# Kernel tuning notes

Measured on AMD Instinct MI355X. Metric: run time of the kernel, lower is better.

Reference implementation:

```python
import jax, jax.numpy as jnp
import numpy as np

B, N, F, D, H, L, K = 128, 128, 13, 256, 8, 8, 10
FF = 2 * D  # FFN / hidden width
HEAD = D // H


def setup_inputs() -> dict:
    key = jax.random.key(0)
    ks = iter(jax.random.split(key, 64))
    def nrm(shape, scale=0.02):
        return jax.random.normal(next(ks), shape, dtype=jnp.float32) * scale
    return {
        "input_features": jax.random.normal(next(ks), (B, N, F), dtype=jnp.float32),
        "input_points": jax.random.normal(next(ks), (B, N, 2), dtype=jnp.float32),
        "input_mask": jnp.ones((B, N, 1), dtype=jnp.float32),
        "input_time": jax.random.uniform(next(ks), (B, 1), dtype=jnp.float32),
        # get_encoding: Dense(2D, gelu) -> Dense(D, gelu)
        "enc_w1": nrm((F, FF)), "enc_b1": jnp.zeros((FF,), jnp.float32),
        "enc_w2": nrm((FF, D)), "enc_b2": jnp.zeros((D,), jnp.float32),
        # FourierProjection MLP (no bias, swish)
        "four_w1": nrm((D, FF)), "four_w2": nrm((FF, D)),
        # FiLM time projection (no bias)
        "time_w": nrm((D, FF)),
        # local KNN MLPs: round 0 input 2*F, round 1 input 2*D
        "loc1_w1": nrm((2 * F, FF)), "loc1_b1": jnp.zeros((FF,), jnp.float32),
        "loc1_w2": nrm((FF, D)), "loc1_b2": jnp.zeros((D,), jnp.float32),
        "loc2_w1": nrm((2 * D, FF)), "loc2_b1": jnp.zeros((FF,), jnp.float32),
        "loc2_w2": nrm((FF, D)), "loc2_b2": jnp.zeros((D,), jnp.float32),
        # transformer encoder layers, stacked over L
        "qkv_w": nrm((L, D, 3 * D)), "qkv_b": jnp.zeros((L, 3 * D), jnp.float32),
        "out_w": nrm((L, D, D)), "out_b": jnp.zeros((L, D), jnp.float32),
        "ln1_g": jnp.ones((L, D), jnp.float32), "ln1_b": jnp.zeros((L, D), jnp.float32),
        "ff1_w": nrm((L, D, FF)), "ff1_b": jnp.zeros((L, FF), jnp.float32),
        "ff2_w": nrm((L, FF, D)), "ff2_b": jnp.zeros((L, D), jnp.float32),
        "gamma": jnp.full((L, D), 1e-5, dtype=jnp.float32),
        "ln2_g": jnp.ones((L, D), jnp.float32), "ln2_b": jnp.zeros((L, D), jnp.float32),
    }


def _ln(x, g, b, eps=1e-5):
    m = jnp.mean(x, axis=-1, keepdims=True)
    v = jnp.var(x, axis=-1, keepdims=True)
    return (x - m) * jax.lax.rsqrt(v + eps) * g + b


def _fourier(t, w1, w2):
    # t: (B,1) -> (B,D)
    half = D // 2
    emb = np.log(10000.0) / (half - 1)
    freq = jnp.exp(-emb * jnp.arange(half, dtype=jnp.float32))
    angle = t * freq[None, :] * 1000.0  # (B, half)
    e = jnp.concatenate([jnp.sin(angle), jnp.cos(angle)], axis=-1)
    e = jax.nn.silu(e @ w1)
    return jax.nn.silu(e @ w2)


def _get_neighbors(points, feats, w1, b1, w2, b2):
    # points: (B,N,P), feats: (B,N,C) -> (B,N,D)
    r = jnp.sum(points * points, axis=-1)  # (B,N)
    d = r[:, :, None] - 2.0 * jnp.einsum('bnp,bmp->bnm', points, points) + r[:, None, :]
    _, idx = jax.lax.top_k(-d, K + 1)
    idx = idx[:, :, 1:]  # drop self, (B,N,K)
    knn = jax.vmap(lambda f, i: f[i])(feats, idx)  # (B,N,K,C)
    center = jnp.broadcast_to(feats[:, :, None, :], knn.shape)
    local = jnp.concatenate([knn - center, center], axis=-1)  # (B,N,K,2C)
    local = jax.nn.gelu(local @ w1 + b1)
    local = jax.nn.gelu(local @ w2 + b2)
    return jnp.mean(local, axis=2)


def _mha(x, mask, wqkv, bqkv, wo, bo):
    Bx, Nx, _ = x.shape
    qkv = x @ wqkv + bqkv
    q, k, v = jnp.split(qkv, 3, axis=-1)
    def heads(t):
        return t.reshape(Bx, Nx, H, HEAD).transpose(0, 2, 1, 3)
    q, k, v = heads(q), heads(k), heads(v)
    scores = jnp.einsum('bhqd,bhkd->bhqk', q, k) * (1.0 / np.sqrt(HEAD))
    keep = mask[:, None, None, :, 0] > 0  # (B,1,1,N)
    scores = jnp.where(keep, scores, -1e9)
    a = jax.nn.softmax(scores, axis=-1)
    o = jnp.einsum('bhqk,bhkd->bhqd', a, v).transpose(0, 2, 1, 3).reshape(Bx, Nx, D)
    return o @ wo + bo


def _pet(input_features, input_points, input_mask, input_time,
         enc_w1, enc_b1, enc_w2, enc_b2, four_w1, four_w2, time_w,
         loc1_w1, loc1_b1, loc1_w2, loc1_b2, loc2_w1, loc2_b1, loc2_w2, loc2_b2,
         qkv_w, qkv_b, out_w, out_b, ln1_g, ln1_b, ff1_w, ff1_b, ff2_w, ff2_b,
         gamma, ln2_g, ln2_b):
    # feature encoding (RandomDrop is identity at eval / feature_drop=0)
    enc = jax.nn.gelu(input_features @ enc_w1 + enc_b1)
    enc = jax.nn.gelu(enc @ enc_w2 + enc_b2)  # (B,N,D)
    # FiLM time conditioning
    t = _fourier(input_time, four_w1, four_w2)  # (B,D)
    t = t[:, None, :] * input_mask  # (B,N,D)
    scale, shift = jnp.split(t @ time_w, 2, axis=-1)
    enc = enc * (1.0 + scale) + shift
    # local KNN aggregation
    coord_shift = 999.0 * (1.0 - input_mask)  # (B,N,1)
    points = input_points[:, :, :2]
    lf = _get_neighbors(coord_shift + points, input_features, loc1_w1, loc1_b1, loc1_w2, loc1_b2)
    lf = _get_neighbors(coord_shift + lf, lf, loc2_w1, loc2_b1, loc2_w2, loc2_b2)
    enc = enc + lf
    skip = enc
    x = enc
    for i in range(L):
        res = x
        a = _mha(x, input_mask, qkv_w[i], qkv_b[i], out_w[i], out_b[i])
        x = _ln(res + a, ln1_g[i], ln1_b[i])
        res = x
        h = jax.nn.gelu(x @ ff1_w[i] + ff1_b[i])
        h = h @ ff2_w[i] + ff2_b[i]
        h = h * gamma[i] * input_mask  # LayerScale with mask
        x = _ln(res + h, ln2_g[i], ln2_b[i])
    return x + skip


def reference(input_features, input_points, input_mask, input_time,
              enc_w1, enc_b1, enc_w2, enc_b2, four_w1, four_w2, time_w,
              loc1_w1, loc1_b1, loc1_w2, loc1_b2, loc2_w1, loc2_b1, loc2_w2, loc2_b2,
              qkv_w, qkv_b, out_w, out_b, ln1_g, ln1_b, ff1_w, ff1_b, ff2_w, ff2_b,
              gamma, ln2_g, ln2_b):
    return _pet(input_features, input_points, input_mask, input_time,
                enc_w1, enc_b1, enc_w2, enc_b2, four_w1, four_w2, time_w,
                loc1_w1, loc1_b1, loc1_w2, loc1_b2, loc2_w1, loc2_b1, loc2_w2, loc2_b2,
                qkv_w, qkv_b, out_w, out_b, ln1_g, ln1_b, ff1_w, ff1_b, ff2_w, ff2_b,
                gamma, ln2_g, ln2_b)
```

## Files before the change

### kernel.cpp

```cpp
#include <hip/hip_runtime.h>
#include <hip/hip_bf16.h>
#include <cmath>

#define DEV_INLINE __device__ __forceinline__

constexpr int Bn = 128;
constexpr int Nn = 128;
constexpr int Fn = 13;
constexpr int Dn = 256;
constexpr int Ln = 8;
constexpr int Kn = 10;
constexpr int FFn = 512;
constexpr int Tn = Bn * Nn;
constexpr int Rn = Tn * Kn;

typedef __attribute__((ext_vector_type(4))) float f32x4;
typedef __attribute__((ext_vector_type(8))) short bf16x8;
typedef unsigned short us;

__device__ float g_x[Tn * Dn];
__device__ float g_skip[Tn * Dn];
__device__ float g_lf2[Tn * Dn];
__device__ float g_dm[Tn * Nn];
__device__ float g_big[Tn * Dn];
__device__ float g_u[Bn * FFn];
__device__ float g_r[Tn];
__device__ float g_pqbias[2048];
__device__ int   g_idx[Rn];
__device__ us g_bigb[Tn * 768];
__device__ us g_xb[Tn * Dn];
__device__ us g_attb[Tn * Dn];
__device__ us g_lf1b[Tn * Dn];
__device__ us g_pq[Tn * 1024];
__device__ us g_h2b[Rn * Dn];
__device__ us g_feat16[Tn * 32];
constexpr int OFF_ENC1 = 0;
constexpr int OFF_ENC2 = OFF_ENC1 + 512 * 32;
constexpr int OFF_W2A  = OFF_ENC2 + 256 * 512;
// ... 18 lines not shown
    return *(us*)&h;
}
DEV_INLINE float blo(unsigned u) { return __uint_as_float(u << 16); }
DEV_INLINE float bhi(unsigned u) { return __uint_as_float(u & 0xFFFF0000u); }
DEV_INLINE unsigned pk2(float a, float b) {
    float2 f; f.x = a; f.y = b;
    __hip_bfloat162 h = __float22bfloat162_rn(f);
    return *(unsigned*)&h;
}

#define GLOAD16(gp, lp)                                                            \
    __builtin_amdgcn_global_load_lds(                                              \
        (const __attribute__((address_space(1))) unsigned int*)(gp),               \
        (__attribute__((address_space(3))) unsigned int*)(lp), 16, 0, 0)

__global__ __launch_bounds__(256) void k_prep(const float* __restrict__ src,
                                              us* __restrict__ dst,
                                              int Kreal, int Kpad, int Nd,
                                              long sstride, long dstride) {
    __shared__ float tile[32][33];
    int l = blockIdx.z;
    const float* s = src + (size_t)l * sstride;
    us* d = dst + (size_t)l * dstride;
    int tid = threadIdx.x;
    int cn = tid & 31, rk = tid >> 5;
    int kbase = blockIdx.y * 32, nbase = blockIdx.x * 32;
#pragma unroll
    for (int p = 0; p < 4; p++) {
        int k = kbase + p * 8 + rk;
        float v = (k < Kreal) ? s[(size_t)k * Nd + nbase + cn] : 0.f;
        tile[p * 8 + rk][cn] = v;
    }
    __syncthreads();
#pragma unroll
    for (int p = 0; p < 4; p++) {
        int nl = p * 8 + rk;
        d[(size_t)(nbase + nl) * Kpad + kbase + cn] = f2b(tile[cn][nl]);
    }
}

__global__ void k_prepPQ(const float* __restrict__ w1, const float* __restrict__ b1,
                         us* __restrict__ dst, float* __restrict__ bdst,
                         int Kreal, int Kpad) {
    int n = blockIdx.x;
    for (int k = threadIdx.x; k < Kpad; k += blockDim.x) {
        float v;
        if (n < 512) v = (k < Kreal) ? w1[(size_t)k * 512 + n] : 0.f;
        else {
            int m = n - 512;
            v = (k < Kreal) ? (w1[(size_t)(Kreal + k) * 512 + m] - w1[(size_t)k * 512 + m]) : 0.f;
        }
        dst[(size_t)n * Kpad + k] = f2b(v);
    }
    if (threadIdx.x == 0) bdst[n] = (n < 512) ? 0.f : b1[n - 512];
}

__global__ void k_featpad(const float* __restrict__ feat, us* __restrict__ fp) {
    int gid = blockIdx.x * 256 + threadIdx.x;
    int t = gid >> 5, c = gid & 31;
    fp[gid] = (c < Fn) ? f2b(feat[(size_t)t * Fn + c]) : (us)0;
}

template <int EPI, bool OBF>
__global__ __launch_bounds__(256) void k_mg2(const us* __restrict__ A,
                                             const us* __restrict__ Bt,
                                             const float* __restrict__ bias,
                                             void* __restrict__ Cp,
                                             int Kd, int Nd) {
    __shared__ __align__(16) us As[128 * 32];
    __shared__ __align__(16) us Bs[128 * 32];
    int tid = threadIdx.x;
    int m0 = blockIdx.y << 7, n0 = blockIdx.x << 7;
    int wave = tid >> 6, lane = tid & 63;
    int wm = (wave & 1) << 6, wn = (wave >> 1) << 6;
    int lm = lane & 15, quad = lane >> 4;
    int r0 = (wave << 5) + (lane >> 2);
    int colu = (lane & 3) << 3;
    const us* pa0 = A + (size_t)(m0 + r0) * Kd + colu;
    const us* pa1 = A + (size_t)(m0 + r0 + 16) * Kd + colu;
    const us* pb0 = Bt + (size_t)(n0 + r0) * Kd + colu;
    const us* pb1 = Bt + (size_t)(n0 + r0 + 16) * Kd + colu;
    auto lAs = (__attribute__((address_space(3))) us*)As;
    auto lBs = (__attribute__((address_space(3))) us*)Bs;
    int lbase = wave << 10;
    f32x4 acc[4][4] = {};
    for (int k0 = 0; k0 < Kd; k0 += 32) {
        __syncthreads();
        GLOAD16(pa0 + k0, lAs + lbase);
        GLOAD16(pa1 + k0, lAs + lbase + 512);
        GLOAD16(pb0 + k0, lBs + lbase);
        GLOAD16(pb1 + k0, lBs + lbase + 512);
        __syncthreads();
        bf16x8 afr[4], bfr[4];
#pragma unroll
        for (int i = 0; i < 4; i++) {
            afr[i] = *(const bf16x8*)&As[(wm + i * 16 + lm) * 32 + (quad << 3)];
            bfr[i] = *(const bf16x8*)&Bs[(wn + i * 16 + lm) * 32 + (quad << 3)];
        }
#pragma unroll
        for (int mf = 0; mf < 4; mf++)
#pragma unroll
            for (int nf = 0; nf < 4; nf++)
                acc[mf][nf] = __builtin_amdgcn_mfma_f32_16x16x32_bf16(afr[mf], bfr[nf], acc[mf][nf], 0, 0, 0);
    }
    float bvs[4];
#pragma unroll
    for (int nf = 0; nf < 4; nf++) bvs[nf] = bias[n0 + wn + nf * 16 + lm];
#pragma unroll
    for (int mf = 0; mf < 4; mf++) {
#pragma unroll
        for (int r = 0; r < 4; r++) {
            size_t row = (size_t)(m0 + wm + mf * 16 + (quad << 2) + r);
// ... 23 lines not shown
                                              us* __restrict__ xbout,
                                              float* __restrict__ finout,
                                              int Kd) {
    __shared__ __align__(16) us As[128 * 32];
    __shared__ __align__(16) us Bs[256 * 32];
    __shared__ float2 part[4][128];
    __shared__ float2 stat[128];
    int tid = threadIdx.x;
    int m0 = blockIdx.x << 7;
    int wave = tid >> 6, lane = tid & 63;
    int wm = (wave & 1) << 6, wn = (wave >> 1) << 6;
    int grp = wave >> 1;
    int lm = lane & 15, quad = lane >> 4;
    int ar = (wave << 4) + (lane >> 2);
    int br = (wave << 5) + (lane >> 2);
    int colu = (lane & 3) << 3;
    const us* pa = A + (size_t)(m0 + ar) * Kd + colu;
    const us* pb0 = Bt + (size_t)br * Kd + colu;
    const us* pb1 = Bt + (size_t)(br + 16) * Kd + colu;
    auto lAs = (__attribute__((address_space(3))) us*)As;
    auto lBs = (__attribute__((address_space(3))) us*)Bs;
    f32x4 acc[4][4] = {};
    for (int k0 = 0; k0 < Kd; k0 += 32) {
        __syncthreads();
        GLOAD16(pa + k0, lAs + (wave << 9));
        GLOAD16(pb0 + k0, lBs + (wave << 10));
        GLOAD16(pb1 + k0, lBs + (wave << 10) + 512);
        __syncthreads();
        bf16x8 afr[4], bfr[4];
#pragma unroll
        for (int i = 0; i < 4; i++) {
            afr[i] = *(const bf16x8*)&As[(wm + i * 16 + lm) * 32 + (quad << 3)];
            bfr[i] = *(const bf16x8*)&Bs[(wn + i * 16 + lm) * 32 + (quad << 3)];
        }
#pragma unroll
        for (int mf = 0; mf < 4; mf++)
#pragma unroll
            for (int nf = 0; nf < 4; nf++)
                acc[mf][nf] = __builtin_amdgcn_mfma_f32_16x16x32_bf16(afr[mf], bfr[nf], acc[mf][nf], 0, 0, 0);
    }
    float bvs[4], gms[4];
#pragma unroll
    for (int nf = 0; nf < 4; nf++) {
        int col = wn + nf * 16 + lm;
        bvs[nf] = bias[col];
        if (PM) gms[nf] = gamma[col];
    }
#pragma unroll
// ... 58 lines not shown
}

__global__ __launch_bounds__(512) void k_knng(const us* __restrict__ pq,
                                              const int* __restrict__ idx,
                                              const us* __restrict__ Bt,
                                              const float* __restrict__ bias,
                                              us* __restrict__ h2b) {
    __shared__ __align__(16) us As[128 * 64];
    __shared__ __align__(16) us Bs[256 * 64];
    int tid = threadIdx.x;
    int m0 = blockIdx.x << 7;
    int wave = tid >> 6, lane = tid & 63;
    int wm = (wave & 1) << 6, wn = (wave >> 1) << 6;
    int lm = lane & 15, quad = lane >> 4;
    int arow = tid >> 2, acolu = (tid & 3) << 4;
    int r = m0 + arow;
    int tok = r / 10;
    int nb = idx[r];
    int prow = (tok & ~127) + nb;
    const us* Pp = pq + (size_t)prow * 1024 + acolu;
    const us* Qp = pq + (size_t)tok * 1024 + 512 + acolu;
    int brow = (wave << 5) + (lane >> 3);
    int bcol = (lane & 7) << 3;
    const us* pb = Bt + (size_t)brow * 512 + bcol;
    auto lBs = (__attribute__((address_space(3))) us*)Bs;
    int lbase = wave << 11;
    f32x4 acc[4][4] = {};
    for (int k0 = 0; k0 < 512; k0 += 64) {
        uint4 pv0 = *(const uint4*)(Pp + k0);
        uint4 pv1 = *(const uint4*)(Pp + k0 + 8);
        uint4 qv0 = *(const uint4*)(Qp + k0);
        uint4 qv1 = *(const uint4*)(Qp + k0 + 8);
        uint4 h0, h1;
        h0.x = pk2(gelu_f(blo(pv0.x) + blo(qv0.x)), gelu_f(bhi(pv0.x) + bhi(qv0.x)));
        h0.y = pk2(gelu_f(blo(pv0.y) + blo(qv0.y)), gelu_f(bhi(pv0.y) + bhi(qv0.y)));
        h0.z = pk2(gelu_f(blo(pv0.z) + blo(qv0.z)), gelu_f(bhi(pv0.z) + bhi(qv0.z)));
        h0.w = pk2(gelu_f(blo(pv0.w) + blo(qv0.w)), gelu_f(bhi(pv0.w) + bhi(qv0.w)));
        h1.x = pk2(gelu_f(blo(pv1.x) + blo(qv1.x)), gelu_f(bhi(pv1.x) + bhi(qv1.x)));
        h1.y = pk2(gelu_f(blo(pv1.y) + blo(qv1.y)), gelu_f(bhi(pv1.y) + bhi(qv1.y)));
        h1.z = pk2(gelu_f(blo(pv1.z) + blo(qv1.z)), gelu_f(bhi(pv1.z) + bhi(qv1.z)));
        h1.w = pk2(gelu_f(blo(pv1.w) + blo(qv1.w)), gelu_f(bhi(pv1.w) + bhi(qv1.w)));
        __syncthreads();
        GLOAD16(pb + k0, lBs + lbase);
        GLOAD16(pb + k0 + 8 * 512, lBs + lbase + 512);
        GLOAD16(pb + k0 + 16 * 512, lBs + lbase + 1024);
        GLOAD16(pb + k0 + 24 * 512, lBs + lbase + 1536);
        *(uint4*)&As[arow * 64 + acolu] = h0;
        *(uint4*)&As[arow * 64 + acolu + 8] = h1;
        __syncthreads();
#pragma unroll
        for (int sub = 0; sub < 2; sub++) {
            bf16x8 afr[4], bfr[4];
#pragma unroll
            for (int i = 0; i < 4; i++) {
                afr[i] = *(const bf16x8*)&As[(wm + i * 16 + lm) * 64 + sub * 32 + (quad << 3)];
                bfr[i] = *(const bf16x8*)&Bs[(wn + i * 16 + lm) * 64 + sub * 32 + (quad << 3)];
            }
#pragma unroll
            for (int mf = 0; mf < 4; mf++)
#pragma unroll
                for (int nf = 0; nf < 4; nf++)
                    acc[mf][nf] = __builtin_amdgcn_mfma_f32_16x16x32_bf16(afr[mf], bfr[nf], acc[mf][nf], 0, 0, 0);
        }
    }
    float bvs[4];
#pragma unroll
    for (int nf = 0; nf < 4; nf++) bvs[nf] = bias[wn + nf * 16 + lm];
#pragma unroll
    for (int mf = 0; mf < 4; mf++) {
#pragma unroll
        for (int rr = 0; rr < 4; rr++) {
// ... 22 lines not shown
        s0 += blo(v.x); s1 += bhi(v.x);
        s2 += blo(v.y); s3 += bhi(v.y);
    }
    s0 *= 0.1f; s1 *= 0.1f; s2 *= 0.1f; s3 *= 0.1f;
    uint2 ob; ob.x = pk2(s0, s1); ob.y = pk2(s2, s3);
    *(uint2*)&lfb[(size_t)t * 256 + c] = ob;
    float sh = 999.f * (1.f - mask[t]);
    float4 w; w.x = s0 + sh; w.y = s1 + sh; w.z = s2 + sh; w.w = s3 + sh;
    *(float4*)&big[(size_t)t * 256 + c] = w;
    float sq = w.x * w.x + w.y * w.y + w.z * w.z + w.w * w.w;
#pragma unroll
    for (int off = 32; off; off >>= 1) sq += __shfl_xor(sq, off, 64);
    if (lane == 0) r[t] = sq;
}

__global__ __launch_bounds__(256) void k_mean2(const us* __restrict__ h2b,
                                               float* __restrict__ lf) {
    int t = blockIdx.x, c = threadIdx.x;
    const us* p = h2b + (size_t)t * Kn * 256 + c;
    float s = 0.f;
#pragma unroll
    for (int k = 0; k < Kn; k++) s += blo((unsigned)p[k * 256]);
    lf[(size_t)t * 256 + c] = s * 0.1f;
}

__global__ __launch_bounds__(256) void k_time(const float* __restrict__ tin,
                                              const float* __restrict__ w1,
                                              const float* __restrict__ w2,
                                              const float* __restrict__ tw,
                                              float* __restrict__ u) {
    __shared__ float e[256], e1[512], t2[256];
    int b = blockIdx.x, tid = threadIdx.x;
    float tv = tin[b];
    if (tid < 128) {
        const float emb = 0.07252236513366287f;
        float fr = expf(-emb * (float)tid);
        float ang = tv * fr * 1000.f;
        e[tid] = sinf(ang);
        e[tid + 128] = cosf(ang);
    }
    __syncthreads();
    for (int j = tid; j < 512; j += 256) {
        float s = 0.f;
        for (int i = 0; i < 256; i++) s += e[i] * w1[(size_t)i * 512 + j];
        e1[j] = s / (1.f + expf(-s));
    }
    __syncthreads();
    {
        float s = 0.f;
        for (int i = 0; i < 512; i++) s += e1[i] * w2[(size_t)i * 256 + tid];
        t2[tid] = s / (1.f + expf(-s));
    }
    __syncthreads();
    for (int j = tid; j < 512; j += 256) {
        float s = 0.f;
        for (int i = 0; i < 256; i++) s += t2[i] * tw[(size_t)i * 512 + j];
        u[(size_t)b * 512 + j] = s;
    }
}

__global__ __launch_bounds__(128) void k_topk2(const float* __restrict__ pts,
                                               const float* __restrict__ mask,
                                               int* __restrict__ idx) {
    int b = blockIdx.x, n = threadIdx.x;
    __shared__ float px[Nn], py[Nn], rr[Nn];
    float shift = 999.f * (1.f - mask[b * Nn + n]);
    float x = pts[(size_t)(b * Nn + n) * 2 + 0] + shift;
    float y = pts[(size_t)(b * Nn + n) * 2 + 1] + shift;
    px[n] = x; py[n] = y; rr[n] = x * x + y * y;
    __syncthreads();
    float rn = rr[n];
    float bd[Kn + 1]; int bi[Kn + 1];
#pragma unroll
    for (int j = 0; j <= Kn; j++) { bd[j] = 3.4e38f; bi[j] = -1; }
    for (int m = 0; m < Nn; m++) {
        float d = rn - 2.f * (x * px[m] + y * py[m]) + rr[m];
        if (d < bd[Kn]) {
            int j = Kn;
            while (j > 0 && d < bd[j - 1]) { bd[j] = bd[j - 1]; bi[j] = bi[j - 1]; j--; }
            bd[j] = d; bi[j] = m;
        }
    }
    for (int j = 1; j <= Kn; j++) idx[(size_t)(b * Nn + n) * Kn + j - 1] = bi[j];
}

__global__ __launch_bounds__(256) void k_dist(const float* __restrict__ fe,
                                              const float* __restrict__ r,
                                              float* __restrict__ Dm) {
    int b = blockIdx.z;
    int m0 = blockIdx.x * 64, n0 = blockIdx.y * 64;
    const float* A = fe + (size_t)b * Nn * Dn;
    __shared__ float As[16][68];
    __shared__ float Bs[16][68];
    int tid = threadIdx.x;
    int tx = tid & 15, ty = tid >> 4;
    int ar = tid >> 2, ac = (tid & 3) << 2;
    float acc[4][4] = {};
    for (int k0 = 0; k0 < Dn; k0 += 16) {
        float4 av = *(const float4*)&A[(size_t)(n0 + ar) * Dn + k0 + ac];
        float4 bv = *(const float4*)&A[(size_t)(m0 + ar) * Dn + k0 + ac];
        __syncthreads();
        As[ac + 0][ar] = av.x; As[ac + 1][ar] = av.y; As[ac + 2][ar] = av.z; As[ac + 3][ar] = av.w;
        Bs[ac + 0][ar] = bv.x; Bs[ac + 1][ar] = bv.y; Bs[ac + 2][ar] = bv.z; Bs[ac + 3][ar] = bv.w;
        __syncthreads();
#pragma unroll
        for (int kk = 0; kk < 16; kk++) {
            float4 a = *(const float4*)&As[kk][ty << 2];
            float4 b2 = *(const float4*)&Bs[kk][tx << 2];
            acc[0][0] += a.x * b2.x; acc[0][1] += a.x * b2.y; acc[0][2] += a.x * b2.z; acc[0][3] += a.x * b2.w;
            acc[1][0] += a.y * b2.x; acc[1][1] += a.y * b2.y; acc[1][2] += a.y * b2.z; acc[1][3] += a.y * b2.w;
            acc[2][0] += a.z * b2.x; acc[2][1] += a.z * b2.y; acc[2][2] += a.z * b2.z; acc[2][3] += a.z * b2.w;
            acc[3][0] += a.w * b2.x; acc[3][1] += a.w * b2.y; acc[3][2] += a.w * b2.z; acc[3][3] += a.w * b2.w;
        }
    }
    float4 rm = *(const float4*)&r[b * Nn + m0 + (tx << 2)];
#pragma unroll
    for (int i = 0; i < 4; i++) {
        int n = n0 + (ty << 2) + i;
        float rn = r[b * Nn + n];
        float4 v;
        v.x = rn - 2.f * acc[i][0] + rm.x;
        v.y = rn - 2.f * acc[i][1] + rm.y;
        v.z = rn - 2.f * acc[i][2] + rm.z;
        v.w = rn - 2.f * acc[i][3] + rm.w;
        *(float4*)&Dm[(size_t)b * Nn * Nn + (size_t)n * Nn + m0 + (tx << 2)] = v;
    }
}

__global__ __launch_bounds__(128) void k_topkg(const float* __restrict__ Dm, int* __restrict__ idx) {
    int b = blockIdx.x, n = threadIdx.x;
    const float* row = Dm + (size_t)b * Nn * Nn + (size_t)n * Nn;
    float bd[Kn + 1]; int bi[Kn + 1];
#pragma unroll
    for (int j = 0; j <= Kn; j++) { bd[j] = 3.4e38f; bi[j] = -1; }
    for (int m = 0; m < Nn; m++) {
        float d = row[m];
        if (d < bd[Kn]) {
            int j = Kn;
            while (j > 0 && d < bd[j - 1]) { bd[j] = bd[j - 1]; bi[j] = bi[j - 1]; j--; }
            bd[j] = d; bi[j] = m;
        }
    }
    for (int j = 1; j <= Kn; j++) idx[(size_t)(b * Nn + n) * Kn + j - 1] = bi[j];
}

__global__ void k_combine(const float* __restrict__ u, const float* __restrict__ mask,
                          const float* __restrict__ lf2, float* __restrict__ x,
                          float* __restrict__ skip, us* __restrict__ xb) {
    int gid = blockIdx.x * 256 + threadIdx.x;
    int t = gid >> 6;
    int c = (gid & 63) << 2;
    int b = t >> 7;
    float m = mask[t];
    float4 xv = *(const float4*)&x[(size_t)t * Dn + c];
    float4 lv = *(const float4*)&lf2[(size_t)t * Dn + c];
    float4 sc = *(const float4*)&u[(size_t)b * 512 + c];
    float4 sh = *(const float4*)&u[(size_t)b * 512 + 256 + c];
    float4 v;
    v.x = xv.x * (1.f + m * sc.x) + m * sh.x + lv.x;
    v.y = xv.y * (1.f + m * sc.y) + m * sh.y + lv.y;
    v.z = xv.z * (1.f + m * sc.z) + m * sh.z + lv.z;
    v.w = xv.w * (1.f + m * sc.w) + m * sh.w + lv.w;
    *(float4*)&x[(size_t)t * Dn + c] = v;
    *(float4*)&skip[(size_t)t * Dn + c] = v;
    uint2 p; p.x = pk2(v.x, v.y); p.y = pk2(v.z, v.w);
    *(uint2*)&xb[(size_t)t * Dn + c] = p;
}

__global__ __launch_bounds__(256) void k_attn(const us* __restrict__ qkv,
                                              const float* __restrict__ mask,
                                              us* __restrict__ outp) {
    __shared__ __align__(16) us Qs[128 * 40];
    __shared__ __align__(16) us Ks[128 * 40];
    __shared__ __align__(16) us Vt[32 * 136];
    __shared__ __align__(16) us Ps[128 * 136];
    __shared__ float msk[128];
    int bh = blockIdx.x;
    int b = bh >> 3, h = bh & 7;
    int tid = threadIdx.x;
    int wave = tid >> 6, lane = tid & 63;
    int lm = lane & 15, quad = lane >> 4;
// ... 121 lines not shown
    const float* qkv_w = (const float*)d_in[19];
    const float* qkv_b = (const float*)d_in[20];
    const float* out_w = (const float*)d_in[21];
    const float* out_b = (const float*)d_in[22];
    const float* ln1g = (const float*)d_in[23];
    const float* ln1b = (const float*)d_in[24];
    const float* ff1w = (const float*)d_in[25];
    const float* ff1b = (const float*)d_in[26];
    const float* ff2w = (const float*)d_in[27];
    const float* ff2b = (const float*)d_in[28];
    const float* gam  = (const float*)d_in[29];
    const float* ln2g = (const float*)d_in[30];
    const float* ln2b = (const float*)d_in[31];
    float* out = (float*)d_out;

    float *x, *skip, *lf2, *dm, *big, *u, *r, *pqbias;
    int* idx;
    us *bigb, *xb, *attb, *lf1b, *pq, *h2b, *feat16, *wt;
    hipGetSymbolAddress((void**)&x,    HIP_SYMBOL(g_x));
    hipGetSymbolAddress((void**)&skip, HIP_SYMBOL(g_skip));
    hipGetSymbolAddress((void**)&lf2,  HIP_SYMBOL(g_lf2));
    hipGetSymbolAddress((void**)&dm,   HIP_SYMBOL(g_dm));
    hipGetSymbolAddress((void**)&big,  HIP_SYMBOL(g_big));
    hipGetSymbolAddress((void**)&u,    HIP_SYMBOL(g_u));
    hipGetSymbolAddress((void**)&r,    HIP_SYMBOL(g_r));
    hipGetSymbolAddress((void**)&pqbias, HIP_SYMBOL(g_pqbias));
    hipGetSymbolAddress((void**)&idx,  HIP_SYMBOL(g_idx));
    hipGetSymbolAddress((void**)&bigb, HIP_SYMBOL(g_bigb));
    hipGetSymbolAddress((void**)&xb,   HIP_SYMBOL(g_xb));
    hipGetSymbolAddress((void**)&attb, HIP_SYMBOL(g_attb));
    hipGetSymbolAddress((void**)&lf1b, HIP_SYMBOL(g_lf1b));
    hipGetSymbolAddress((void**)&pq,   HIP_SYMBOL(g_pq));
    hipGetSymbolAddress((void**)&h2b,  HIP_SYMBOL(g_h2b));
    hipGetSymbolAddress((void**)&feat16, HIP_SYMBOL(g_feat16));
    hipGetSymbolAddress((void**)&wt,   HIP_SYMBOL(g_wt));

    k_prep<<<dim3(16, 1, 1), 256, 0, stream>>>(enc_w1, wt + OFF_ENC1, 13, 32, 512, 0, 0);
    k_prep<<<dim3(8, 16, 1), 256, 0, stream>>>(enc_w2, wt + OFF_ENC2, 512, 512, 256, 0, 0);
    k_prep<<<dim3(8, 16, 1), 256, 0, stream>>>(l1w2, wt + OFF_W2A, 512, 512, 256, 0, 0);
    k_prep<<<dim3(8, 16, 1), 256, 0, stream>>>(l2w2, wt + OFF_W2B, 512, 512, 256, 0, 0);
    k_prepPQ<<<1024, 64, 0, stream>>>(l1w1, l1b1, wt + OFF_PQ1, pqbias, 13, 32);
    k_prepPQ<<<1024, 256, 0, stream>>>(l2w1, l2b1, wt + OFF_PQ2, pqbias + 1024, 256, 256);
    k_prep<<<dim3(24, 8, 8), 256, 0, stream>>>(qkv_w, wt + OFF_QKV, 256, 256, 768, 256 * 768, 768 * 256);
    k_prep<<<dim3(8, 8, 8), 256, 0, stream>>>(out_w, wt + OFF_OUT, 256, 256, 256, 256 * 256, 256 * 256);
    k_prep<<<dim3(16, 8, 8), 256, 0, stream>>>(ff1w, wt + OFF_FF1, 256, 256, 512, 256 * 512, 512 * 256);
    k_prep<<<dim3(8, 16, 8), 256, 0, stream>>>(ff2w, wt + OFF_FF2, 512, 512, 256, 512 * 256, 256 * 512);
    k_featpad<<<Tn * 32 / 256, 256, 0, stream>>>(f_feat, feat16);

    k_time<<<Bn, 256, 0, stream>>>(f_time, four_w1, four_w2, time_w, u);
    k_mg2<1, true><<<dim3(4, 128), 256, 0, stream>>>(feat16, wt + OFF_ENC1, enc_b1, bigb, 32, 512);
    k_mg2<1, false><<<dim3(2, 128), 256, 0, stream>>>(bigb, wt + OFF_ENC2, enc_b2, x, 512, 256);
    k_topk2<<<Bn, Nn, 0, stream>>>(f_pts, f_mask, idx);
    k_mg2<0, true><<<dim3(8, 128), 256, 0, stream>>>(feat16, wt + OFF_PQ1, pqbias, pq, 32, 1024);
    k_knng<<<Rn / 128, 512, 0, stream>>>(pq, idx, wt + OFF_W2A, l1b2, h2b);
    k_mean1s<<<Tn, 64, 0, stream>>>(h2b, f_mask, lf1b, big, r);
    k_dist<<<dim3(2, 2, Bn), 256, 0, stream>>>(big, r, dm);
    k_topkg<<<Bn, Nn, 0, stream>>>(dm, idx);
    k_mg2<0, true><<<dim3(8, 128), 256, 0, stream>>>(lf1b, wt + OFF_PQ2, pqbias + 1024, pq, 256, 1024);
    k_knng<<<Rn / 128, 512, 0, stream>>>(pq, idx, wt + OFF_W2B, l2b2, h2b);
    k_mean2<<<Tn, 256, 0, stream>>>(h2b, lf2);
    k_combine<<<Tn * 64 / 256, 256, 0, stream>>>(u, f_mask, lf2, x, skip, xb);
    for (int l = 0; l < Ln; l++) {
        k_mg2<0, true><<<dim3(6, 128), 256, 0, stream>>>(
            xb, wt + OFF_QKV + (size_t)l * 768 * 256, qkv_b + l * 768, bigb, 256, 768);
        k_attn<<<Bn * 8, 256, 0, stream>>>(bigb, f_mask, attb);
        k_mgln<false, false><<<128, 512, 0, stream>>>(
            attb, wt + OFF_OUT + (size_t)l * 256 * 256, out_b + l * 256,
            x, nullptr, f_mask, ln1g + l * Dn, ln1b + l * Dn, nullptr, x, xb, nullptr, 256);
        k_mg2<1, true><<<dim3(4, 128), 256, 0, stream>>>(
            xb, wt + OFF_FF1 + (size_t)l * 512 * 256, ff1b + l * 512, bigb, 256, 512);
        if (l < Ln - 1)
            k_mgln<true, false><<<128, 512, 0, stream>>>(
                bigb, wt + OFF_FF2 + (size_t)l * 256 * 512, ff2b + l * 256,
                x, gam + l * Dn, f_mask, ln2g + l * Dn, ln2b + l * Dn, nullptr, x, xb, nullptr, 512);
        else
            k_mgln<true, true><<<128, 512, 0, stream>>>(
// ... 5 lines not shown
```

Measured before the change: 1.488 ms.

## Fuse prep kernels, swizzle LDS layouts, merge distance+topk and mean+combine

Merges all weight-prep, feature padding, time-embedding and first KNN kernels into a single multi-segment launch. It adds an XOR swizzle to the LDS tiles in the MFMA GEMM kernels to reduce bank conflicts. The second-round distance matrix and top-k are fused into one per-batch kernel that keeps the distance matrix in shared memory, and the neighbour mean is fused with the FiLM combine. This cuts launches and global round-trips, at the cost of a larger heterogeneous prep kernel and a heavier k_dtop block.

```diff
diff --git a/kernel.cpp b/kernel.cpp
--- a/kernel.cpp
+++ b/kernel.cpp
@@ -20,8 +20,6 @@
 
 __device__ float g_x[Tn * Dn];
 __device__ float g_skip[Tn * Dn];
-__device__ float g_lf2[Tn * Dn];
-__device__ float g_dm[Tn * Nn];
 __device__ float g_big[Tn * Dn];
 __device__ float g_u[Bn * FFn];
 __device__ float g_r[Tn];
@@ -70,36 +68,49 @@
         (const __attribute__((address_space(1))) unsigned int*)(gp),               \
         (__attribute__((address_space(3))) unsigned int*)(lp), 16, 0, 0)
 
-__global__ __launch_bounds__(256) void k_prep(const float* __restrict__ src,
-                                              us* __restrict__ dst,
-                                              int Kreal, int Kpad, int Nd,
-                                              long sstride, long dstride) {
-    __shared__ float tile[32][33];
-    int l = blockIdx.z;
-    const float* s = src + (size_t)l * sstride;
-    us* d = dst + (size_t)l * dstride;
-    int tid = threadIdx.x;
+constexpr int UP0 = 0;
+constexpr int UP1 = UP0 + 16;
+constexpr int UP2 = UP1 + 128;
+constexpr int UP3 = UP2 + 128;
+constexpr int UP4 = UP3 + 128;
+constexpr int UP5 = UP4 + 1536;
+constexpr int UP6 = UP5 + 512;
+constexpr int UP7 = UP6 + 1024;
+constexpr int UP8 = UP7 + 1024;
+constexpr int UP9 = UP8 + 1024;
+constexpr int UP10 = UP9 + 1024;
+constexpr int UP11 = UP10 + 2048;
+constexpr int UP12 = UP11 + 128;
+constexpr int UPN = UP12 + 128;
+
+DEV_INLINE void prep_seg(const float* __restrict__ src, us* __restrict__ dst,
+                         int Kreal, int Kpad, int Nd, long sstride, long dstride,
+                         int gx, int gy, int lb, int tid, float* tile) {
+    int z = lb / (gx * gy);
+    int rem = lb - z * gx * gy;
+    int by = rem / gx, bx = rem - by * gx;
+    const float* s = src + (size_t)z * sstride;
+    us* d = dst + (size_t)z * dstride;
     int cn = tid & 31, rk = tid >> 5;
-    int kbase = blockIdx.y * 32, nbase = blockIdx.x * 32;
+    int kbase = by * 32, nbase = bx * 32;
 #pragma unroll
     for (int p = 0; p < 4; p++) {
         int k = kbase + p * 8 + rk;
         float v = (k < Kreal) ? s[(size_t)k * Nd + nbase + cn] : 0.f;
-        tile[p * 8 + rk][cn] = v;
+        tile[(p * 8 + rk) * 33 + cn] = v;
     }
     __syncthreads();
 #pragma unroll
     for (int p = 0; p < 4; p++) {
         int nl = p * 8 + rk;
-        d[(size_t)(nbase + nl) * Kpad + kbase + cn] = f2b(tile[cn][nl]);
-    }
-}
-
-__global__ void k_prepPQ(const float* __restrict__ w1, const float* __restrict__ b1,
-                         us* __restrict__ dst, float* __restrict__ bdst,
-                         int Kreal, int Kpad) {
-    int n = blockIdx.x;
-    for (int k = threadIdx.x; k < Kpad; k += blockDim.x) {
+        d[(size_t)(nbase + nl) * Kpad + kbase + cn] = f2b(tile[cn * 33 + nl]);
+    }
+}
+
+DEV_INLINE void prepPQ_seg(const float* __restrict__ w1, const float* __restrict__ b1,
+                           us* __restrict__ dst, float* __restrict__ bdst,
+                           int Kreal, int Kpad, int n, int tid) {
+    for (int k = tid; k < Kpad; k += 256) {
         float v;
         if (n < 512) v = (k < Kreal) ? w1[(size_t)k * 512 + n] : 0.f;
         else {
@@ -108,13 +119,105 @@
         }
         dst[(size_t)n * Kpad + k] = f2b(v);
     }
-    if (threadIdx.x == 0) bdst[n] = (n < 512) ? 0.f : b1[n - 512];
-}
-
-__global__ void k_featpad(const float* __restrict__ feat, us* __restrict__ fp) {
-    int gid = blockIdx.x * 256 + threadIdx.x;
-    int t = gid >> 5, c = gid & 31;
-    fp[gid] = (c < Fn) ? f2b(feat[(size_t)t * Fn + c]) : (us)0;
+    if (tid == 0) bdst[n] = (n < 512) ? 0.f : b1[n - 512];
+}
+
+__global__ __launch_bounds__(256) void k_uprep(
+    const float* __restrict__ enc_w1, const float* __restrict__ enc_w2,
+    const float* __restrict__ l1w2, const float* __restrict__ l2w2,
+    const float* __restrict__ qkv_w, const float* __restrict__ out_w,
+    const float* __restrict__ ff1w, const float* __restrict__ ff2w,
+    const float* __restrict__ l1w1, const float* __restrict__ l1b1,
+    const float* __restrict__ l2w1, const float* __restrict__ l2b1,
+    const float* __restrict__ feat, const float* __restrict__ tin,
+    const float* __restrict__ four_w1, const float* __restrict__ four_w2,
+    const float* __restrict__ time_w, const float* __restrict__ pts,
+    const float* __restrict__ mask,
+    us* __restrict__ wt, float* __restrict__ pqbias, us* __restrict__ fp,
+    float* __restrict__ u, int* __restrict__ idx) {
+    __shared__ float shmem[1056];
+    int b = blockIdx.x, tid = threadIdx.x;
+    if (b < UP1) {
+        prep_seg(enc_w1, wt + OFF_ENC1, 13, 32, 512, 0, 0, 16, 1, b - UP0, tid, shmem);
+    } else if (b < UP2) {
+        prep_seg(enc_w2, wt + OFF_ENC2, 512, 512, 256, 0, 0, 8, 16, b - UP1, tid, shmem);
+    } else if (b < UP3) {
+        prep_seg(l1w2, wt + OFF_W2A, 512, 512, 256, 0, 0, 8, 16, b - UP2, tid, shmem);
+    } else if (b < UP4) {
+        prep_seg(l2w2, wt + OFF_W2B, 512, 512, 256, 0, 0, 8, 16, b - UP3, tid, shmem);
+    } else if (b < UP5) {
+        prep_seg(qkv_w, wt + OFF_QKV, 256, 256, 768, 256 * 768, 768 * 256, 24, 8, b - UP4, tid, shmem);
+    } else if (b < UP6) {
+        prep_seg(out_w, wt + OFF_OUT, 256, 256, 256, 256 * 256, 256 * 256, 8, 8, b - UP5, tid, shmem);
+    } else if (b < UP7) {
+        prep_seg(ff1w, wt + OFF_FF1, 256, 256, 512, 256 * 512, 512 * 256, 16, 8, b - UP6, tid, shmem);
+    } else if (b < UP8) {
+        prep_seg(ff2w, wt + OFF_FF2, 512, 512, 256, 512 * 256, 256 * 512, 8, 16, b - UP7, tid, shmem);
+    } else if (b < UP9) {
+        prepPQ_seg(l1w1, l1b1, wt + OFF_PQ1, pqbias, 13, 32, b - UP8, tid);
+    } else if (b < UP10) {
+        prepPQ_seg(l2w1, l2b1, wt + OFF_PQ2, pqbias + 1024, 256, 256, b - UP9, tid);
+    } else if (b < UP11) {
+        int gid = (b - UP10) * 256 + tid;
+        int t = gid >> 5, c = gid & 31;
+        fp[gid] = (c < Fn) ? f2b(feat[(size_t)t * Fn + c]) : (us)0;
+    } else if (b < UP12) {
+        float* e = shmem; float* e1 = shmem + 256; float* t2 = shmem + 768;
+        int bb = b - UP11;
+        float tv = tin[bb];
+        if (tid < 128) {
+            const float emb = 0.07252236513366287f;
+            float fr = expf(-emb * (float)tid);
+            float ang = tv * fr * 1000.f;
+            e[tid] = sinf(ang);
+            e[tid + 128] = cosf(ang);
+        }
+        __syncthreads();
+        for (int j = tid; j < 512; j += 256) {
+            float s = 0.f;
+            for (int i = 0; i < 256; i++) s += e[i] * four_w1[(size_t)i * 512 + j];
+            e1[j] = s / (1.f + expf(-s));
+        }
+        __syncthreads();
+        {
+            float s = 0.f;
+            for (int i = 0; i < 512; i++) s += e1[i] * four_w2[(size_t)i * 256 + tid];
+            t2[tid] = s / (1.f + expf(-s));
+        }
+        __syncthreads();
+        for (int j = tid; j < 512; j += 256) {
+            float s = 0.f;
+            for (int i = 0; i < 256; i++) s += t2[i] * time_w[(size_t)i * 512 + j];
+            u[(size_t)bb * 512 + j] = s;
+        }
+    } else {
+        float* px = shmem; float* py = shmem + 128; float* rr = shmem + 256;
+        int bb = b - UP12;
+        if (tid < 128) {
+            int n = tid;
+            float shift = 999.f * (1.f - mask[bb * Nn + n]);
+            float x = pts[(size_t)(bb * Nn + n) * 2 + 0] + shift;
+            float y = pts[(size_t)(bb * Nn + n) * 2 + 1] + shift;
+            px[n] = x; py[n] = y; rr[n] = x * x + y * y;
+        }
+        __syncthreads();
+        if (tid < 128) {
+            int n = tid;
+            float x = px[n], y = py[n], rn = rr[n];
+            float bd[Kn + 1]; int bi[Kn + 1];
+#pragma unroll
+            for (int j = 0; j <= Kn; j++) { bd[j] = 3.4e38f; bi[j] = -1; }
+            for (int m = 0; m < Nn; m++) {
+                float d = rn - 2.f * (x * px[m] + y * py[m]) + rr[m];
+                if (d < bd[Kn]) {
+                    int j = Kn;
+                    while (j > 0 && d < bd[j - 1]) { bd[j] = bd[j - 1]; bi[j] = bi[j - 1]; j--; }
+                    bd[j] = d; bi[j] = m;
+                }
+            }
+            for (int j = 1; j <= Kn; j++) idx[(size_t)(bb * Nn + n) * Kn + j - 1] = bi[j];
+        }
+    }
 }
 
 template <int EPI, bool OBF>
@@ -131,7 +234,7 @@
     int wm = (wave & 1) << 6, wn = (wave >> 1) << 6;
     int lm = lane & 15, quad = lane >> 4;
     int r0 = (wave << 5) + (lane >> 2);
-    int colu = (lane & 3) << 3;
+    int colu = (((lane & 3) ^ ((lane >> 2) & 3)) << 3);
     const us* pa0 = A + (size_t)(m0 + r0) * Kd + colu;
     const us* pa1 = A + (size_t)(m0 + r0 + 16) * Kd + colu;
     const us* pb0 = Bt + (size_t)(n0 + r0) * Kd + colu;
@@ -139,6 +242,7 @@
     auto lAs = (__attribute__((address_space(3))) us*)As;
     auto lBs = (__attribute__((address_space(3))) us*)Bs;
     int lbase = wave << 10;
+    int fcol = ((quad ^ (lm & 3)) << 3);
     f32x4 acc[4][4] = {};
     for (int k0 = 0; k0 < Kd; k0 += 32) {
         __syncthreads();
@@ -150,8 +254,8 @@
         bf16x8 afr[4], bfr[4];
 #pragma unroll
         for (int i = 0; i < 4; i++) {
-            afr[i] = *(const bf16x8*)&As[(wm + i * 16 + lm) * 32 + (quad << 3)];
-            bfr[i] = *(const bf16x8*)&Bs[(wn + i * 16 + lm) * 32 + (quad << 3)];
+            afr[i] = *(const bf16x8*)&As[(wm + i * 16 + lm) * 32 + fcol];
+            bfr[i] = *(const bf16x8*)&Bs[(wn + i * 16 + lm) * 32 + fcol];
         }
 #pragma unroll
         for (int mf = 0; mf < 4; mf++)
@@ -205,12 +309,13 @@
     int lm = lane & 15, quad = lane >> 4;
     int ar = (wave << 4) + (lane >> 2);
     int br = (wave << 5) + (lane >> 2);
-    int colu = (lane & 3) << 3;
+    int colu = (((lane & 3) ^ ((lane >> 2) & 3)) << 3);
     const us* pa = A + (size_t)(m0 + ar) * Kd + colu;
     const us* pb0 = Bt + (size_t)br * Kd + colu;
     const us* pb1 = Bt + (size_t)(br + 16) * Kd + colu;
     auto lAs = (__attribute__((address_space(3))) us*)As;
     auto lBs = (__attribute__((address_space(3))) us*)Bs;
+    int fcol = ((quad ^ (lm & 3)) << 3);
     f32x4 acc[4][4] = {};
     for (int k0 = 0; k0 < Kd; k0 += 32) {
         __syncthreads();
@@ -221,8 +326,8 @@
         bf16x8 afr[4], bfr[4];
 #pragma unroll
         for (int i = 0; i < 4; i++) {
-            afr[i] = *(const bf16x8*)&As[(wm + i * 16 + lm) * 32 + (quad << 3)];
-            bfr[i] = *(const bf16x8*)&Bs[(wn + i * 16 + lm) * 32 + (quad << 3)];
+            afr[i] = *(const bf16x8*)&As[(wm + i * 16 + lm) * 32 + fcol];
+            bfr[i] = *(const bf16x8*)&Bs[(wn + i * 16 + lm) * 32 + fcol];
         }
 #pragma unroll
         for (int mf = 0; mf < 4; mf++)
@@ -311,6 +416,8 @@
     int wm = (wave & 1) << 6, wn = (wave >> 1) << 6;
     int lm = lane & 15, quad = lane >> 4;
     int arow = tid >> 2, acolu = (tid & 3) << 4;
+    int asw = arow & 7;
+    int ablk0 = ((tid & 3) << 1) ^ asw, ablk1 = (((tid & 3) << 1) + 1) ^ asw;
     int r = m0 + arow;
     int tok = r / 10;
     int nb = idx[r];
@@ -318,10 +425,11 @@
     const us* Pp = pq + (size_t)prow * 1024 + acolu;
     const us* Qp = pq + (size_t)tok * 1024 + 512 + acolu;
     int brow = (wave << 5) + (lane >> 3);
-    int bcol = (lane & 7) << 3;
+    int bcol = (((lane & 7) ^ (lane >> 3)) << 3);
     const us* pb = Bt + (size_t)brow * 512 + bcol;
     auto lBs = (__attribute__((address_space(3))) us*)Bs;
     int lbase = wave << 11;
+    int fsw = lm & 7;
     f32x4 acc[4][4] = {};
     for (int k0 = 0; k0 < 512; k0 += 64) {
         uint4 pv0 = *(const uint4*)(Pp + k0);
@@ -342,16 +450,18 @@
         GLOAD16(pb + k0 + 8 * 512, lBs + lbase + 512);
         GLOAD16(pb + k0 + 16 * 512, lBs + lbase + 1024);
         GLOAD16(pb + k0 + 24 * 512, lBs + lbase + 1536);
-        *(uint4*)&As[arow * 64 + acolu] = h0;
-        *(uint4*)&As[arow * 64 + acolu + 8] = h1;
+        *(uint4*)&As[arow * 64 + (ablk0 << 3)] = h0;
+        *(uint4*)&As[arow * 64 + (ablk1 << 3)] = h1;
         __syncthreads();
 #pragma unroll
         for (int sub = 0; sub < 2; sub++) {
+            int lblk = (sub << 2) + quad;
+            int fcol = ((lblk ^ fsw) << 3);
             bf16x8 afr[4], bfr[4];
 #pragma unroll
             for (int i = 0; i < 4; i++) {
-                afr[i] = *(const bf16x8*)&As[(wm + i * 16 + lm) * 64 + sub * 32 + (quad << 3)];
-                bfr[i] = *(const bf16x8*)&Bs[(wn + i * 16 + lm) * 64 + sub * 32 + (quad << 3)];
+                afr[i] = *(const bf16x8*)&As[(wm + i * 16 + lm) * 64 + fcol];
+                bfr[i] = *(const bf16x8*)&Bs[(wn + i * 16 + lm) * 64 + fcol];
             }
 #pragma unroll
             for (int mf = 0; mf < 4; mf++)
@@ -404,157 +514,88 @@
     if (lane == 0) r[t] = sq;
 }
 
-__global__ __launch_bounds__(256) void k_mean2(const us* __restrict__ h2b,
-                                               float* __restrict__ lf) {
+__global__ __launch_bounds__(256) void k_dtop(const float* __restrict__ big,
+                                              const float* __restrict__ r,
+                                              int* __restrict__ idx) {
+    __shared__ float Dm[128][132];
+    __shared__ float At[16][132];
+    int b = blockIdx.x, tid = threadIdx.x;
+    int tx = tid & 15, ty = tid >> 4;
+    const float* A = big + (size_t)b * Nn * Dn;
+    float acc[8][8] = {};
+    int srow = tid >> 1, sc8 = (tid & 1) << 3;
+    for (int k0 = 0; k0 < 256; k0 += 16) {
+        float4 v0 = *(const float4*)&A[(size_t)srow * 256 + k0 + sc8];
+        float4 v1 = *(const float4*)&A[(size_t)srow * 256 + k0 + sc8 + 4];
+        __syncthreads();
+        At[sc8 + 0][srow] = v0.x; At[sc8 + 1][srow] = v0.y;
+        At[sc8 + 2][srow] = v0.z; At[sc8 + 3][srow] = v0.w;
+        At[sc8 + 4][srow] = v1.x; At[sc8 + 5][srow] = v1.y;
+        At[sc8 + 6][srow] = v1.z; At[sc8 + 7][srow] = v1.w;
+        __syncthreads();
+#pragma unroll
+        for (int kk = 0; kk < 16; kk++) {
+            float av[8], bv[8];
+#pragma unroll
+            for (int i = 0; i < 8; i++) av[i] = At[kk][ty * 8 + i];
+#pragma unroll
+            for (int j = 0; j < 8; j++) bv[j] = At[kk][tx * 8 + j];
+#pragma unroll
+            for (int i = 0; i < 8; i++)
+#pragma unroll
+                for (int j = 0; j < 8; j++) acc[i][j] += av[i] * bv[j];
+        }
+    }
+    __syncthreads();
+#pragma unroll
+    for (int i = 0; i < 8; i++) {
+        int n = ty * 8 + i;
+        float rn = r[b * Nn + n];
+#pragma unroll
+        for (int j = 0; j < 8; j++) {
+            int m = tx * 8 + j;
+            Dm[n][m] = rn - 2.f * acc[i][j] + r[b * Nn + m];
+        }
+    }
+    __syncthreads();
+    if (tid < 128) {
+        int n = tid;
+        float bd[Kn + 1]; int bi[Kn + 1];
+#pragma unroll
+        for (int j = 0; j <= Kn; j++) { bd[j] = 3.4e38f; bi[j] = -1; }
+        for (int m = 0; m < Nn; m++) {
+            float d = Dm[n][m];
+            if (d < bd[Kn]) {
+                int j = Kn;
+                while (j > 0 && d < bd[j - 1]) { bd[j] = bd[j - 1]; bi[j] = bi[j - 1]; j--; }
+                bd[j] = d; bi[j] = m;
+            }
+        }
+        for (int j = 1; j <= Kn; j++) idx[(size_t)(b * Nn + n) * Kn + j - 1] = bi[j];
+    }
+}
+
+__global__ __launch_bounds__(256) void k_meanc(const us* __restrict__ h2b,
+                                               const float* __restrict__ u,
+                                               const float* __restrict__ mask,
+                                               float* __restrict__ x,
+                                               float* __restrict__ skip,
+                                               us* __restrict__ xb) {
     int t = blockIdx.x, c = threadIdx.x;
     const us* p = h2b + (size_t)t * Kn * 256 + c;
     float s = 0.f;
 #pragma unroll
     for (int k = 0; k < Kn; k++) s += blo((unsigned)p[k * 256]);
-    lf[(size_t)t * 256 + c] = s * 0.1f;
-}
-
-__global__ __launch_bounds__(256) void k_time(const float* __restrict__ tin,
-                                              const float* __restrict__ w1,
-                                              const float* __restrict__ w2,
-                                              const float* __restrict__ tw,
-                                              float* __restrict__ u) {
-    __shared__ float e[256], e1[512], t2[256];
-    int b = blockIdx.x, tid = threadIdx.x;
-    float tv = tin[b];
-    if (tid < 128) {
-        const float emb = 0.07252236513366287f;
-        float fr = expf(-emb * (float)tid);
-        float ang = tv * fr * 1000.f;
-        e[tid] = sinf(ang);
-        e[tid + 128] = cosf(ang);
-    }
-    __syncthreads();
-    for (int j = tid; j < 512; j += 256) {
-        float s = 0.f;
-        for (int i = 0; i < 256; i++) s += e[i] * w1[(size_t)i * 512 + j];
-        e1[j] = s / (1.f + expf(-s));
-    }
-    __syncthreads();
-    {
-        float s = 0.f;
-        for (int i = 0; i < 512; i++) s += e1[i] * w2[(size_t)i * 256 + tid];
-        t2[tid] = s / (1.f + expf(-s));
-    }
-    __syncthreads();
-    for (int j = tid; j < 512; j += 256) {
-        float s = 0.f;
-        for (int i = 0; i < 256; i++) s += t2[i] * tw[(size_t)i * 512 + j];
-        u[(size_t)b * 512 + j] = s;
-    }
-}
-
-__global__ __launch_bounds__(128) void k_topk2(const float* __restrict__ pts,
-                                               const float* __restrict__ mask,
-                                               int* __restrict__ idx) {
-    int b = blockIdx.x, n = threadIdx.x;
-    __shared__ float px[Nn], py[Nn], rr[Nn];
-    float shift = 999.f * (1.f - mask[b * Nn + n]);
-    float x = pts[(size_t)(b * Nn + n) * 2 + 0] + shift;
-    float y = pts[(size_t)(b * Nn + n) * 2 + 1] + shift;
-    px[n] = x; py[n] = y; rr[n] = x * x + y * y;
-    __syncthreads();
-    float rn = rr[n];
-    float bd[Kn + 1]; int bi[Kn + 1];
-#pragma unroll
-    for (int j = 0; j <= Kn; j++) { bd[j] = 3.4e38f; bi[j] = -1; }
-    for (int m = 0; m < Nn; m++) {
-        float d = rn - 2.f * (x * px[m] + y * py[m]) + rr[m];
-        if (d < bd[Kn]) {
-            int j = Kn;
-            while (j > 0 && d < bd[j - 1]) { bd[j] = bd[j - 1]; bi[j] = bi[j - 1]; j--; }
-            bd[j] = d; bi[j] = m;
-        }
-    }
-    for (int j = 1; j <= Kn; j++) idx[(size_t)(b * Nn + n) * Kn + j - 1] = bi[j];
-}
-
-__global__ __launch_bounds__(256) void k_dist(const float* __restrict__ fe,
-                                              const float* __restrict__ r,
-                                              float* __restrict__ Dm) {
-    int b = blockIdx.z;
-    int m0 = blockIdx.x * 64, n0 = blockIdx.y * 64;
-    const float* A = fe + (size_t)b * Nn * Dn;
-    __shared__ float As[16][68];
-    __shared__ float Bs[16][68];
-    int tid = threadIdx.x;
-    int tx = tid & 15, ty = tid >> 4;
-    int ar = tid >> 2, ac = (tid & 3) << 2;
-    float acc[4][4] = {};
-    for (int k0 = 0; k0 < Dn; k0 += 16) {
-        float4 av = *(const float4*)&A[(size_t)(n0 + ar) * Dn + k0 + ac];
-        float4 bv = *(const float4*)&A[(size_t)(m0 + ar) * Dn + k0 + ac];
-        __syncthreads();
-        As[ac + 0][ar] = av.x; As[ac + 1][ar] = av.y; As[ac + 2][ar] = av.z; As[ac + 3][ar] = av.w;
-        Bs[ac + 0][ar] = bv.x; Bs[ac + 1][ar] = bv.y; Bs[ac + 2][ar] = bv.z; Bs[ac + 3][ar] = bv.w;
-        __syncthreads();
-#pragma unroll
-        for (int kk = 0; kk < 16; kk++) {
-            float4 a = *(const float4*)&As[kk][ty << 2];
-            float4 b2 = *(const float4*)&Bs[kk][tx << 2];
-            acc[0][0] += a.x * b2.x; acc[0][1] += a.x * b2.y; acc[0][2] += a.x * b2.z; acc[0][3] += a.x * b2.w;
-            acc[1][0] += a.y * b2.x; acc[1][1] += a.y * b2.y; acc[1][2] += a.y * b2.z; acc[1][3] += a.y * b2.w;
-            acc[2][0] += a.z * b2.x; acc[2][1] += a.z * b2.y; acc[2][2] += a.z * b2.z; acc[2][3] += a.z * b2.w;
-            acc[3][0] += a.w * b2.x; acc[3][1] += a.w * b2.y; acc[3][2] += a.w * b2.z; acc[3][3] += a.w * b2.w;
-        }
-    }
-    float4 rm = *(const float4*)&r[b * Nn + m0 + (tx << 2)];
-#pragma unroll
-    for (int i = 0; i < 4; i++) {
-        int n = n0 + (ty << 2) + i;
-        float rn = r[b * Nn + n];
-        float4 v;
-        v.x = rn - 2.f * acc[i][0] + rm.x;
-        v.y = rn - 2.f * acc[i][1] + rm.y;
-        v.z = rn - 2.f * acc[i][2] + rm.z;
-        v.w = rn - 2.f * acc[i][3] + rm.w;
-        *(float4*)&Dm[(size_t)b * Nn * Nn + (size_t)n * Nn + m0 + (tx << 2)] = v;
-    }
-}
-
-__global__ __launch_bounds__(128) void k_topkg(const float* __restrict__ Dm, int* __restrict__ idx) {
-    int b = blockIdx.x, n = threadIdx.x;
-    const float* row = Dm + (size_t)b * Nn * Nn + (size_t)n * Nn;
-    float bd[Kn + 1]; int bi[Kn + 1];
-#pragma unroll
-    for (int j = 0; j <= Kn; j++) { bd[j] = 3.4e38f; bi[j] = -1; }
-    for (int m = 0; m < Nn; m++) {
-        float d = row[m];
-        if (d < bd[Kn]) {
-            int j = Kn;
-            while (j > 0 && d < bd[j - 1]) { bd[j] = bd[j - 1]; bi[j] = bi[j - 1]; j--; }
-            bd[j] = d; bi[j] = m;
-        }
-    }
-    for (int j = 1; j <= Kn; j++) idx[(size_t)(b * Nn + n) * Kn + j - 1] = bi[j];
-}
-
-__global__ void k_combine(const float* __restrict__ u, const float* __restrict__ mask,
-                          const float* __restrict__ lf2, float* __restrict__ x,
-                          float* __restrict__ skip, us* __restrict__ xb) {
-    int gid = blockIdx.x * 256 + threadIdx.x;
-    int t = gid >> 6;
-    int c = (gid & 63) << 2;
+    s *= 0.1f;
     int b = t >> 7;
     float m = mask[t];
-    float4 xv = *(const float4*)&x[(size_t)t * Dn + c];
-    float4 lv = *(const float4*)&lf2[(size_t)t * Dn + c];
-    float4 sc = *(const float4*)&u[(size_t)b * 512 + c];
-    float4 sh = *(const float4*)&u[(size_t)b * 512 + 256 + c];
-    float4 v;
-    v.x = xv.x * (1.f + m * sc.x) + m * sh.x + lv.x;
-    v.y = xv.y * (1.f + m * sc.y) + m * sh.y + lv.y;
-    v.z = xv.z * (1.f + m * sc.z) + m * sh.z + lv.z;
-    v.w = xv.w * (1.f + m * sc.w) + m * sh.w + lv.w;
-    *(float4*)&x[(size_t)t * Dn + c] = v;
-    *(float4*)&skip[(size_t)t * Dn + c] = v;
-    uint2 p; p.x = pk2(v.x, v.y); p.y = pk2(v.z, v.w);
-    *(uint2*)&xb[(size_t)t * Dn + c] = p;
+    float xv = x[(size_t)t * Dn + c];
+    float sc = u[(size_t)b * 512 + c];
+    float sh = u[(size_t)b * 512 + 256 + c];
+    float v = xv * (1.f + m * sc) + m * sh + s;
+    x[(size_t)t * Dn + c] = v;
+    skip[(size_t)t * Dn + c] = v;
+    xb[(size_t)t * Dn + c] = f2b(v);
 }
 
 __global__ __launch_bounds__(256) void k_attn(const us* __restrict__ qkv,
@@ -706,13 +747,11 @@
     const float* ln2b = (const float*)d_in[31];
     float* out = (float*)d_out;
 
-    float *x, *skip, *lf2, *dm, *big, *u, *r, *pqbias;
+    float *x, *skip, *big, *u, *r, *pqbias;
     int* idx;
     us *bigb, *xb, *attb, *lf1b, *pq, *h2b, *feat16, *wt;
     hipGetSymbolAddress((void**)&x,    HIP_SYMBOL(g_x));
     hipGetSymbolAddress((void**)&skip, HIP_SYMBOL(g_skip));
-    hipGetSymbolAddress((void**)&lf2,  HIP_SYMBOL(g_lf2));
-    hipGetSymbolAddress((void**)&dm,   HIP_SYMBOL(g_dm));
     hipGetSymbolAddress((void**)&big,  HIP_SYMBOL(g_big));
     hipGetSymbolAddress((void**)&u,    HIP_SYMBOL(g_u));
     hipGetSymbolAddress((void**)&r,    HIP_SYMBOL(g_r));
@@ -727,31 +766,20 @@
     hipGetSymbolAddress((void**)&feat16, HIP_SYMBOL(g_feat16));
     hipGetSymbolAddress((void**)&wt,   HIP_SYMBOL(g_wt));
 
-    k_prep<<<dim3(16, 1, 1), 256, 0, stream>>>(enc_w1, wt + OFF_ENC1, 13, 32, 512, 0, 0);
-    k_prep<<<dim3(8, 16, 1), 256, 0, stream>>>(enc_w2, wt + OFF_ENC2, 512, 512, 256, 0, 0);
-    k_prep<<<dim3(8, 16, 1), 256, 0, stream>>>(l1w2, wt + OFF_W2A, 512, 512, 256, 0, 0);
-    k_prep<<<dim3(8, 16, 1), 256, 0, stream>>>(l2w2, wt + OFF_W2B, 512, 512, 256, 0, 0);
-    k_prepPQ<<<1024, 64, 0, stream>>>(l1w1, l1b1, wt + OFF_PQ1, pqbias, 13, 32);
-    k_prepPQ<<<1024, 256, 0, stream>>>(l2w1, l2b1, wt + OFF_PQ2, pqbias + 1024, 256, 256);
-    k_prep<<<dim3(24, 8, 8), 256, 0, stream>>>(qkv_w, wt + OFF_QKV, 256, 256, 768, 256 * 768, 768 * 256);
-    k_prep<<<dim3(8, 8, 8), 256, 0, stream>>>(out_w, wt + OFF_OUT, 256, 256, 256, 256 * 256, 256 * 256);
-    k_prep<<<dim3(16, 8, 8), 256, 0, stream>>>(ff1w, wt + OFF_FF1, 256, 256, 512, 256 * 512, 512 * 256);
-    k_prep<<<dim3(8, 16, 8), 256, 0, stream>>>(ff2w, wt + OFF_FF2, 512, 512, 256, 512 * 256, 256 * 512);
-    k_featpad<<<Tn * 32 / 256, 256, 0, stream>>>(f_feat, feat16);
-
-    k_time<<<Bn, 256, 0, stream>>>(f_time, four_w1, four_w2, time_w, u);
+    k_uprep<<<UPN, 256, 0, stream>>>(
+        enc_w1, enc_w2, l1w2, l2w2, qkv_w, out_w, ff1w, ff2w,
+        l1w1, l1b1, l2w1, l2b1, f_feat, f_time, four_w1, four_w2, time_w,
+        f_pts, f_mask, wt, pqbias, feat16, u, idx);
+
     k_mg2<1, true><<<dim3(4, 128), 256, 0, stream>>>(feat16, wt + OFF_ENC1, enc_b1, bigb, 32, 512);
     k_mg2<1, false><<<dim3(2, 128), 256, 0, stream>>>(bigb, wt + OFF_ENC2, enc_b2, x, 512, 256);
-    k_topk2<<<Bn, Nn, 0, stream>>>(f_pts, f_mask, idx);
     k_mg2<0, true><<<dim3(8, 128), 256, 0, stream>>>(feat16, wt + OFF_PQ1, pqbias, pq, 32, 1024);
     k_knng<<<Rn / 128, 512, 0, stream>>>(pq, idx, wt + OFF_W2A, l1b2, h2b);
     k_mean1s<<<Tn, 64, 0, stream>>>(h2b, f_mask, lf1b, big, r);
-    k_dist<<<dim3(2, 2, Bn), 256, 0, stream>>>(big, r, dm);
-    k_topkg<<<Bn, Nn, 0, stream>>>(dm, idx);
+    k_dtop<<<Bn, 256, 0, stream>>>(big, r, idx);
     k_mg2<0, true><<<dim3(8, 128), 256, 0, stream>>>(lf1b, wt + OFF_PQ2, pqbias + 1024, pq, 256, 1024);
     k_knng<<<Rn / 128, 512, 0, stream>>>(pq, idx, wt + OFF_W2B, l2b2, h2b);
-    k_mean2<<<Tn, 256, 0, stream>>>(h2b, lf2);
-    k_combine<<<Tn * 64 / 256, 256, 0, stream>>>(u, f_mask, lf2, x, skip, xb);
+    k_meanc<<<Tn, 256, 0, stream>>>(h2b, u, f_mask, x, skip, xb);
     for (int l = 0; l < Ln; l++) {
         k_mg2<0, true><<<dim3(6, 128), 256, 0, stream>>>(
             xb, wt + OFF_QKV + (size_t)l * 768 * 256, qkv_b + l * 768, bigb, 256, 768);
```

New measurement: 1.572 ms. 1.06x slower.
